# Kernel optimization log

Measured on AMD Instinct MI355X. Metric: run time of the kernel, lower is better.

Reference implementation:

```python
import jax, jax.numpy as jnp
import numpy as np

CR = 64                      # cond_repeat
DILS = tuple(2 ** i for _ in range(2) for i in range(10))  # 2 blocks x 10 layers
Q_ZERO = 128


def setup_inputs() -> dict:
    key = jax.random.key(0)
    B, C, TE = 8, 64, 8          # batch, cond channels, encoding timesteps
    R, S, Q = 128, 128, 256      # residual, skip, classes
    L = len(DILS)
    ks = jax.random.split(key, 12)
    sc = 0.1
    return {
        "encodings": jax.random.normal(ks[0], (B, C, TE), jnp.float32),
        "first_w": jax.random.normal(ks[1], (R, 1, 2), jnp.float32) * sc,
        "first_b": jnp.zeros((R,), jnp.float32),
        "causal_w": jax.random.normal(ks[2], (L, 2 * R, R, 2), jnp.float32) * sc,
        "causal_b": jnp.zeros((L, 2 * R), jnp.float32),
        "cond_w": jax.random.normal(ks[3], (L, 2 * R, C), jnp.float32) * sc,
        "cond_b": jnp.zeros((L, 2 * R), jnp.float32),
        "res_w": jax.random.normal(ks[4], (L, R, R), jnp.float32) * sc,
        "res_b": jnp.zeros((L, R), jnp.float32),
        "skip_w": jax.random.normal(ks[5], (L, S, R), jnp.float32) * sc,
        "skip_b": jnp.zeros((L, S), jnp.float32),
        "skipc_w": jax.random.normal(ks[6], (S, R), jnp.float32) * sc,
        "skipc_b": jnp.zeros((S,), jnp.float32),
        "fc_w": jax.random.normal(ks[7], (S, S), jnp.float32) * sc,
        "fc_b": jnp.zeros((S,), jnp.float32),
        "condf_w": jax.random.normal(ks[8], (S, C), jnp.float32) * sc,
        "condf_b": jnp.zeros((S,), jnp.float32),
        "logits_w": jax.random.normal(ks[9], (Q, S), jnp.float32) * sc,
        "logits_b": jnp.zeros((Q,), jnp.float32),
    }


def _generate(encodings, first_w, first_b, causal_w, causal_b, cond_w, cond_b,
              res_w, res_b, skip_w, skip_b, skipc_w, skipc_b, fc_w, fc_b,
              condf_w, condf_b, logits_w, logits_b):
    B = encodings.shape[0]
    R = res_w.shape[1]
    T = encodings.shape[2] * CR

    # ring buffers emulate QueuedConv1d (queue length = dilation, zero-initialized)
    buf_first0 = jnp.zeros((B, 1), jnp.float32)
    bufs0 = tuple(jnp.zeros((B, d, R), jnp.float32) for d in DILS)
    sample0 = jnp.full((B,), Q_ZERO, jnp.int32)

    def step(carry, t):
        sample, buf_first, bufs = carry
        x = sample.astype(jnp.float32) / 255.0 - 0.5                      # [B]
        c = jax.lax.dynamic_index_in_dim(encodings, t // CR, axis=2,
                                         keepdims=False)                  # [B,C]
        # first causal conv (1 -> R, kernel 2): tap0 on delayed sample, tap1 on current
        prev0 = buf_first[:, 0]
        buf_first = buf_first.at[:, 0].set(x)
        res = (prev0[:, None] * first_w[None, :, 0, 0]
               + x[:, None] * first_w[None, :, 0, 1] + first_b)           # [B,R]
        skip = res @ skipc_w.T + skipc_b                                  # [B,S]
        new_bufs = []
        for l, d in enumerate(DILS):
            idx = jnp.mod(t, d)
            prev = jax.lax.dynamic_index_in_dim(bufs[l], idx, axis=1, keepdims=False)
            new_bufs.append(jax.lax.dynamic_update_index_in_dim(bufs[l], res, idx, axis=1))
            z = (prev @ causal_w[l, :, :, 0].T + res @ causal_w[l, :, :, 1].T
                 + causal_b[l] + c @ cond_w[l].T + cond_b[l])             # [B,2R]
            gate, out = jnp.split(z, 2, axis=1)
            h = jax.nn.sigmoid(gate) * jnp.tanh(out)                      # [B,R]
            res = res + h @ res_w[l].T + res_b[l]
            skip = skip + h @ skip_w[l].T + skip_b[l]
        s = jax.nn.relu(skip) @ fc_w.T + fc_b + c @ condf_w.T + condf_b
        logits = jax.nn.relu(s) @ logits_w.T + logits_b                   # [B,Q]
        sample = jnp.argmax(logits, axis=1).astype(jnp.int32)             # 'max' sampling
        return (sample, buf_first, tuple(new_bufs)), (sample, logits)

    _, (samples, logits) = jax.lax.scan(step, (sample0, buf_first0, bufs0),
                                        jnp.arange(T))
    return samples, logits  # [T,B] int32, [T,B,Q] float32


def reference(encodings, first_w, first_b, causal_w, causal_b, cond_w, cond_b,
              res_w, res_b, skip_w, skip_b, skipc_w, skipc_b, fc_w, fc_b,
              condf_w, condf_b, logits_w, logits_b):
    return _generate(encodings, first_w, first_b, causal_w, causal_b, cond_w, cond_b,
                     res_w, res_b, skip_w, skip_b, skipc_w, skipc_b, fc_w, fc_b,
                     condf_w, condf_b, logits_w, logits_b)
```

## Files before the change

kernel.cpp:

```cpp
#include <hip/hip_runtime.h>
#include <math.h>

#define BB 8
#define TT 512
#define LL 20
#define NBLK 64
#define NTHR 256

typedef float f4 __attribute__((ext_vector_type(4)));
typedef unsigned long long ull;

__constant__ int c_dil[LL] = {1,2,4,8,16,32,64,128,256,512,
                              1,2,4,8,16,32,64,128,256,512};
__constant__ int c_roff[LL] = {-1,0,4096,12288,28672,61440,126976,258048,520192,1044480,
                               2093056,2095104,2099200,2107392,2123776,2156544,
                               2222080,2353152,2615296,3139584};

constexpr size_t OFF_RING = 0;
constexpr size_t OFF_X    = 4188160;

#define P_WC     0
#define P_F      20480
#define P_WST    30208
#define P_WSKIPC 30720
#define P_WFC    30976
#define P_WLOG   31232
#define P_WF0    31744
#define P_WF1    31872
#define P_FB     32000
#define P_CONDZ  32128
#define P_SFC    32768
#define P_RESB   32784
#define P_SKIPB  32824
#define P_ZB     32864
#define P_LOGB   32944
#define P_SKIPCB 32948
#define P_Z0C    32952
#define P_SKC    32976
#define P_XS     32984
#define P_SZ     33008
#define P_SL     33040
#define P_SKACC  33072
#define P_R2     33088
#define P_CF     33104
#define P_PREVF  33632
#define P_HF     34688
#define P_RESF   35744
#define P_RES0   36800
#define POOL_FL  37856

__device__ __forceinline__ f4 ldx(const f4* p) {
    f4 r;
    asm volatile("global_load_dwordx4 %0, %1, off sc0 sc1\n\ts_waitcnt vmcnt(0)"
                 : "=v"(r) : "v"(p) : "memory");
    return r;
}
__device__ __forceinline__ void ldx2(const f4* p0, const f4* p1, f4& a, f4& b) {
    asm volatile("global_load_dwordx4 %0, %2, off sc0 sc1\n\t"
                 "global_load_dwordx4 %1, %3, off sc0 sc1\n\t"
                 "s_waitcnt vmcnt(0)"
                 : "=v"(a), "=v"(b) : "v"(p0), "v"(p1) : "memory");
}
__device__ __forceinline__ void ld4x(const f4* a0, const f4* a1, const f4* a2, const f4* a3,
                                     f4& r0, f4& r1, f4& r2, f4& r3) {
    asm volatile("global_load_dwordx4 %0, %4, off sc0 sc1\n\t"
                 "global_load_dwordx4 %1, %5, off sc0 sc1\n\t"
                 "global_load_dwordx4 %2, %6, off sc0 sc1\n\t"
                 "global_load_dwordx4 %3, %7, off sc0 sc1\n\t"
                 "s_waitcnt vmcnt(0)"
                 : "=v"(r0), "=v"(r1), "=v"(r2), "=v"(r3)
                 : "v"(a0), "v"(a1), "v"(a2), "v"(a3) : "memory");
}
__device__ __forceinline__ void stx(f4* p, f4 v) {
    asm volatile("global_store_dwordx4 %0, %1, off sc0 sc1"
                 :: "v"(p), "v"(v) : "memory");
}
__device__ __forceinline__ void spin(const f4* p, int e, f4& a) {
    while (__float_as_int(a.w) != e) a = ldx(p);
}

__device__ __forceinline__ float pick16(const float* sl, int V) {
    if (V < 8) return sl[V];
    if (V >= 9 && V < 17) return sl[V - 1];
    return 0.f;
}
__device__ __forceinline__ void publish16(f4* slot, int J, const float* sl, int e) {
    if (threadIdx.x < 6) {
        int q = threadIdx.x;
        f4 v;
        v.x = pick16(sl, 3*q);
        v.y = pick16(sl, 3*q + 1);
        v.z = pick16(sl, 3*q + 2);
        v.w = __int_as_float(e);
        stx(slot + J*6 + q, v);
    }
}
__device__ __forceinline__ void publish_half(f4* slot, int J, int r, const float* half8,
                                             int e, int m) {
    int base = 3*m;
    f4 v;
    v.x = half8[base];
    v.y = (base + 1 < 8) ? half8[base + 1] : 0.f;
    v.z = (base + 2 < 8) ? half8[base + 2] : 0.f;
    v.w = __int_as_float(e);
    stx(slot + J*6 + 3*r + m, v);
}
__device__ __forceinline__ void scat16(float* dst, f4 v, int vi, bool dorelu) {
    int j = vi / 6, q = vi - 6*j;
    #pragma unroll
    for (int i = 0; i < 3; ++i) {
        int V = 3*q + i;
        float x = v[i];
        if (dorelu) x = fmaxf(x, 0.f);
        if (V < 8)                 dst[V*132 + 2*j]           = x;
        else if (V >= 9 && V < 17) dst[(V - 9)*132 + 2*j + 1] = x;
    }
}
__device__ __forceinline__ void consume16(const f4* slot, int e, float* dst, bool dorelu) {
    int m = threadIdx.x;
    const f4 *p0 = slot + m, *p1 = slot + 256 + m;
    f4 a, b;
    bool two = (m < 128);
    if (two) ldx2(p0, p1, a, b); else a = ldx(p0);
    spin(p0, e, a);
    if (two) spin(p1, e, b);
    scat16(dst, a, m, dorelu);
    if (two) scat16(dst, b, m + 256, dorelu);
}
__device__ __forceinline__ void consume_pair(const f4* sR, int eR, float* dR,
                                             const f4* sH, int eH, float* dH) {
    int m = threadIdx.x;
    const f4 *pra = sR + m, *prb = sR + 256 + m, *pha = sH + m, *phb = sH + 256 + m;
    f4 ra, rb, ha, hb;
    bool two = (m < 128);
    if (two) ld4x(pra, prb, pha, phb, ra, rb, ha, hb);
    else     ldx2(pra, pha, ra, ha);
    spin(pra, eR, ra);
    if (two) spin(prb, eR, rb);
    scat16(dR, ra, m, false);
    if (two) scat16(dR, rb, m + 256, false);
    spin(pha, eH, ha);
    if (two) spin(phb, eH, hb);
    scat16(dH, ha, m, false);
    if (two) scat16(dH, hb, m + 256, false);
}

__global__ __launch_bounds__(NTHR, 1) void wn_gen(
    const float* __restrict__ enc,
    const float* __restrict__ first_w,  const float* __restrict__ first_b,
    const float* __restrict__ causal_w, const float* __restrict__ causal_b,
    const float* __restrict__ cond_w,   const float* __restrict__ cond_b,
    const float* __restrict__ res_w,    const float* __restrict__ res_b,
    const float* __restrict__ skip_w,   const float* __restrict__ skip_b,
    const float* __restrict__ skipc_w,  const float* __restrict__ skipc_b,
    const float* __restrict__ fc_w,     const float* __restrict__ fc_b,
    const float* __restrict__ condf_w,  const float* __restrict__ condf_b,
    const float* __restrict__ logits_w, const float* __restrict__ logits_b,
    float* __restrict__ wsf, float* __restrict__ out)
{
    extern __shared__ float pool[];
    const int tid = threadIdx.x;
    const int J = blockIdx.x;
    float* ring = wsf + OFF_RING;
    f4* xb = (f4*)(wsf + OFF_X);

    for (int m = tid; m < 20480; m += NTHR) {
        int l = m >> 10, rem = m & 1023, g = rem >> 8, i = rem & 255;
        int grow = (g < 2) ? (2*J + g) : (128 + 2*J + (g - 2));
        int col = i & 127, k = i >> 7;
        pool[P_WC + m] = causal_w[((size_t)(l*256 + grow)*128 + col)*2 + k];
    }
    if (tid < 256) {
        int r = tid >> 7, i = tid & 127;
        pool[P_WSKIPC + tid] = skipc_w[(size_t)(2*J + r)*128 + i];
        pool[P_WFC + tid]    = fc_w[(size_t)(2*J + r)*128 + i];
    }
    for (int m = tid; m < 512; m += NTHR) {
        int w = m >> 7, i = m & 127;
        pool[P_WLOG + m] = logits_w[(size_t)(4*J + w)*128 + i];
    }
    if (tid < 128) {
        pool[P_WF0 + tid] = first_w[2*tid];
        pool[P_WF1 + tid] = first_w[2*tid + 1];
        pool[P_FB + tid]  = first_b[tid];
    }
    if (tid < 40) {
        int l = tid >> 1, r = tid & 1;
        pool[P_RESB + tid]  = res_b[l*128 + 2*J + r];
        pool[P_SKIPB + tid] = skip_b[l*128 + 2*J + r];
    }
    if (tid < 4) pool[P_LOGB + tid] = logits_b[4*J + tid];
    if (tid < 2) pool[P_SKIPCB + tid] = skipc_b[2*J + tid];
    if (tid < 8) {
        pool[P_XS + tid]      = 128.f/255.f - 0.5f;
        pool[P_XS + 8 + tid]  = 0.f;
        pool[P_XS + 16 + tid] = 0.f;
    }
    __syncthreads();

    for (int l = 0; l < 19; ++l) {
        for (int m = tid; m < 512; m += NTHR) {
            int g = m >> 7, j = m & 127;
            const float* w1 = pool + P_WC + ((l+1)*4 + g)*256 + 128;
            const float* rw = res_w + (size_t)l*128*128 + j;
            float acc = 0.f;
            #pragma unroll 8
            for (int i = 0; i < 128; ++i) acc += w1[i] * rw[(size_t)i*128];
            pool[P_F + (l*4 + g)*128 + j] = acc;
        }
    }
    if (tid < 80) {
        int l = tid >> 2, g = tid & 3;
        float acc = 0.f;
        if (l >= 1) {
            const float* w1 = pool + P_WC + (l*4 + g)*256 + 128;
            for (int i = 0; i < 128; ++i) acc += w1[i] * res_b[(l-1)*128 + i];
        }
        pool[P_ZB + tid] = acc;
    }
    if (tid < 4) {
        const float* w0 = pool + P_WC + tid*256;
        const float* w1 = w0 + 128;
        float kp = 0.f, kc = 0.f, u = 0.f, c1 = 0.f, a0 = 0.f;
        for (int j = 0; j < 128; ++j) {
            float f0 = pool[P_WF0 + j], f1 = pool[P_WF1 + j], fbv = pool[P_FB + j];
            kp += w0[j]*fbv; kc += w1[j]*fbv;
            u  += w0[j]*f0;  c1 += w0[j]*f1 + w1[j]*f0;  a0 += w1[j]*f1;
        }
        pool[P_Z0C + tid*6 + 0] = kp;
        pool[P_Z0C + tid*6 + 1] = kc;
        pool[P_Z0C + tid*6 + 2] = u;
        pool[P_Z0C + tid*6 + 3] = c1;
        pool[P_Z0C + tid*6 + 4] = a0;
    }
    if (tid < 2) {
        const float* wr = pool + P_WSKIPC + tid*128;
        float sk = pool[P_SKIPCB + tid], sa = 0.f, sb = 0.f;
        for (int j = 0; j < 128; ++j) {
            sk += wr[j]*pool[P_FB + j];
            sa += wr[j]*pool[P_WF0 + j];
            sb += wr[j]*pool[P_WF1 + j];
        }
        pool[P_SKC + tid*3 + 0] = sk;
        pool[P_SKC + tid*3 + 1] = sa;
        pool[P_SKC + tid*3 + 2] = sb;
    }
    __syncthreads();

    int e = 0;
    int er_pending = 0;
    int esk = 0;

    for (int t = 0; t < TT; ++t) {
        if ((t & 63) == 0) {
            int te = t >> 6;
            for (int m = tid; m < 512; m += NTHR) {
                int b = m >> 6, j = m & 63;
                pool[P_CF + b*66 + j] = enc[(size_t)b*512 + j*8 + te];
            }
            __syncthreads();
            for (int m = tid; m < 640; m += NTHR) {
                int l = m >> 5, rem = m & 31, g = rem >> 3, b = rem & 7;
                int grow = (g < 2) ? (2*J + g) : (128 + 2*J + (g - 2));
                float acc = causal_b[l*256 + grow] + cond_b[l*256 + grow]
                          + pool[P_ZB + l*4 + g];
                const float* cw = cond_w + (size_t)(l*256 + grow)*64;
                const float* cf = pool + P_CF + b*66;
                for (int j = 0; j < 64; ++j) acc += cw[j]*cf[j];
                pool[P_CONDZ + l*32 + g*8 + b] = acc;
            }
            if (tid < 16) {
                int r = tid >> 3, b = tid & 7, row = 2*J + r;
                float acc = fc_b[row] + condf_b[row];
                const float* cw = condf_w + (size_t)row*64;
                const float* cf = pool + P_CF + b*66;
                for (int j = 0; j < 64; ++j) acc += cw[j]*cf[j];
                pool[P_SFC + r*8 + b] = acc;
            }
            __syncthreads();
        }

        ++e; const int eh0 = e;
        {
            if (tid < 16) {
                int r = tid & 1, b = tid >> 1;
                float kf  = (t >= 1) ? 1.f : 0.f;
                float x0v = pool[P_XS + b];
                float x1v = pool[P_XS + 8 + b];
                float x2v = pool[P_XS + 16 + b];
                const float* zc = pool + P_Z0C;
                int g0 = r, g1 = 2 + r;
                float zg = kf*zc[g0*6+0] + zc[g0*6+1] + x2v*zc[g0*6+2]
                         + x1v*zc[g0*6+3] + x0v*zc[g0*6+4] + pool[P_CONDZ + g0*8 + b];
                float zo = kf*zc[g1*6+0] + zc[g1*6+1] + x2v*zc[g1*6+2]
                         + x1v*zc[g1*6+3] + x0v*zc[g1*6+4] + pool[P_CONDZ + g1*8 + b];
                pool[P_SL + r*8 + b] = (1.f/(1.f + expf(-zg))) * tanhf(zo);
            }
            publish16(xb + (size_t)(eh0 & 3)*768, J, pool + P_SL, eh0);
        }
        for (int m = tid; m < 1024; m += NTHR) {
            int b = m >> 7, r = m & 127;
            pool[P_RES0 + b*132 + r] =
                pool[P_FB + r] + pool[P_XS + 8 + b]*pool[P_WF0 + r]
                               + pool[P_XS + b]    *pool[P_WF1 + r];
        }
        if (tid < 16) {
            int r = tid >> 3, b = tid & 7;
            float x0v = pool[P_XS + b], x1v = pool[P_XS + 8 + b];
            pool[P_SKACC + r*8 + b] = pool[P_SKC + r*3] + x1v*pool[P_SKC + r*3 + 1]
                                                        + x0v*pool[P_SKC + r*3 + 2];
            int row = 2*J + r;
            pool[P_R2 + r*8 + b] = pool[P_FB + row] + x1v*pool[P_WF0 + row]
                                                    + x0v*pool[P_WF1 + row];
        }

        for (int l = 0; l < LL; ++l) {
            int ehh;
            if (l == 0) {
                ehh = eh0;
            } else {
                {
                    int g = tid >> 6, lane = tid & 63, b = lane >> 3, k = lane & 7;
                    const float* w0 = pool + P_WC + (l*4 + g)*256;
                    const float* pv = pool + P_PREVF + b*132;
                    const float* rs = ((l == 1) ? pool + P_RES0 : pool + P_RESF) + b*132;
                    const float* fm = pool + P_F + ((l-1)*4 + g)*128;
                    const float* hh = pool + P_HF + b*132;
                    float acc = 0.f;
                    #pragma unroll
                    for (int i = 0; i < 16; ++i) {
                        int j = k + 8*i;
                        acc += w0[j]*pv[j] + w0[128 + j]*rs[j] + fm[j]*hh[j];
                    }
                    acc += __shfl_xor(acc,1); acc += __shfl_xor(acc,2); acc += __shfl_xor(acc,4);
                    if (k == 0) pool[P_SZ + g*8 + b] = acc;
                }
                __syncthreads();
                ++e; ehh = e;
                if (tid < 16) {
                    int r = tid & 1, b = tid >> 1;
                    float g = pool[P_SZ + r*8 + b]     + pool[P_CONDZ + l*32 + r*8 + b];
                    float o = pool[P_SZ + (2+r)*8 + b] + pool[P_CONDZ + l*32 + (2+r)*8 + b];
                    pool[P_SL + r*8 + b] = (1.f/(1.f + expf(-g))) * tanhf(o);
                }
                publish16(xb + (size_t)(ehh & 3)*768, J, pool + P_SL, ehh);
            }
            float wv0, wv1;
            {
                int r0 = tid >> 7, i0 = tid & 127;
                wv0 = res_w [(size_t)(l*128 + 2*J + r0)*128 + i0];
                wv1 = skip_w[(size_t)(l*128 + 2*J + r0)*128 + i0];
            }
            ull pfa = 0, pfb = 0;
            if (l <= 18) {
                int d = c_dil[l+1];
                if (t >= d) {
                    int slot = (t - d) & (2*d - 1);
                    const float* rp = ring + c_roff[l+1] + (size_t)slot*1024 + tid*4;
                    pfa = __hip_atomic_load((const ull*)rp,     __ATOMIC_RELAXED, __HIP_MEMORY_SCOPE_AGENT);
                    pfb = __hip_atomic_load((const ull*)(rp+2), __ATOMIC_RELAXED, __HIP_MEMORY_SCOPE_AGENT);
                }
            }
            if (l == 0) {
                consume16(xb + (size_t)(ehh & 3)*768, ehh, pool + P_HF, false);
            } else if (l <= 18) {
                consume_pair(xb + (size_t)(er_pending & 3)*768, er_pending, pool + P_RESF,
                             xb + (size_t)(ehh & 3)*768,        ehh,        pool + P_HF);
            } else {
                consume16(xb + (size_t)(ehh & 3)*768, ehh, pool + P_HF, false);
            }
            pool[P_WST + tid] = wv0;
            pool[P_WST + 256 + tid] = wv1;
            __syncthreads();
            {
                int w = tid >> 6, lane = tid & 63, b = lane >> 3, k = lane & 7;
                int r = w & 1, isSkip = w >> 1;
                if (isSkip || l <= 18) {
                    const float* wr = pool + P_WST + (isSkip ? 256 : 0) + r*128;
                    const float* hh = pool + P_HF + b*132;
                    float acc = 0.f;
                    #pragma unroll
                    for (int i = 0; i < 16; ++i) { int j = k + 8*i; acc += wr[j]*hh[j]; }
                    acc += __shfl_xor(acc,1); acc += __shfl_xor(acc,2); acc += __shfl_xor(acc,4);
                    if (k == 0) {
                        if (isSkip) {
                            pool[P_SKACC + r*8 + b] += acc + pool[P_SKIPB + l*2 + r];
                        } else {
                            float v = pool[P_R2 + r*8 + b] + acc + pool[P_RESB + l*2 + r];
                            pool[P_R2 + r*8 + b] = v;
                            pool[P_SL + r*8 + b] = v;
                            int d = c_dil[l+1];
                            int slot = t & (2*d - 1);
                            float* wp = ring + c_roff[l+1] + (size_t)slot*1024 + b*128 + 2*J + r;
                            __hip_atomic_store(wp, v, __ATOMIC_RELAXED, __HIP_MEMORY_SCOPE_AGENT);
                        }
                    }
                }
            }
            {
                int w = tid >> 6, lane = tid & 63;
                if (l <= 17) {
                    ++e; er_pending = e;
                    if (w < 2 && lane < 3)
                        publish_half(xb + (size_t)(e & 3)*768, J, w,
                                     pool + P_SL + w*8, e, lane);
                } else if (l == 19) {
                    ++e; esk = e;
                    if (w >= 2 && lane < 3)
                        publish_half(xb + (size_t)(e & 3)*768, J, w - 2,
                                     pool + P_SKACC + (w - 2)*8, e, lane);
                }
            }
            if (l <= 18) {
                int b = tid >> 5, c = (tid & 31)*4;
                union { ull u; float f[2]; } u0, u1;
                u0.u = pfa; u1.u = pfb;
                float* dp = pool + P_PREVF + b*132 + c;
                dp[0] = u0.f[0]; dp[1] = u0.f[1]; dp[2] = u1.f[0]; dp[3] = u1.f[1];
            }
            __syncthreads();
        }

        consume16(xb + (size_t)(esk & 3)*768, esk, pool + P_HF, false);
        __syncthreads();
        {
            int w = tid >> 6, lane = tid & 63, b = lane >> 3, k = lane & 7;
            if (w < 2) {
                const float* wr = pool + P_WFC + w*128;
                const float* sk = pool + P_HF + b*132;
                float acc = 0.f;
                #pragma unroll
                for (int i = 0; i < 16; ++i) { int j = k + 8*i; acc += wr[j]*fmaxf(sk[j], 0.f); }
                acc += __shfl_xor(acc,1); acc += __shfl_xor(acc,2); acc += __shfl_xor(acc,4);
                if (k == 0) pool[P_SL + w*8 + b] = acc + pool[P_SFC + w*8 + b];
            }
        }
        ++e;
        {
            int w = tid >> 6, lane = tid & 63;
            if (w < 2 && lane < 3)
                publish_half(xb + (size_t)(e & 3)*768, J, w, pool + P_SL + w*8, e, lane);
        }
        consume16(xb + (size_t)(e & 3)*768, e, pool + P_RESF, true);
        __syncthreads();
        {
            int b = tid >> 5, g = (tid >> 3) & 3, k = tid & 7;
            const float* wr = pool + P_WLOG + g*128;
            const float* sv = pool + P_RESF + b*132;
            float acc = 0.f;
            #pragma unroll
            for (int i = 0; i < 16; ++i) { int j = k + 8*i; acc += wr[j]*sv[j]; }
            acc += __shfl_xor(acc,1); acc += __shfl_xor(acc,2); acc += __shfl_xor(acc,4);
            float v = acc + pool[P_LOGB + g];
            float best = (k == 0) ? v : -3.4e38f;
            int bi = 4*J + g;
            { float ov = __shfl_xor(best, 8);  int oi = __shfl_xor(bi, 8);
              if (ov > best || (ov == best && oi < bi)) { best = ov; bi = oi; } }
            { float ov = __shfl_xor(best, 16); int oi = __shfl_xor(bi, 16);
              if (ov > best || (ov == best && oi < bi)) { best = ov; bi = oi; } }
            if (k == 0) out[4096 + ((size_t)(t*BB + b))*256 + 4*J + g] = v;
            if ((tid & 31) == 0) { pool[P_SL + b] = best; pool[P_SL + 8 + b] = (float)bi; }
        }
        __syncthreads();
        ++e;
        publish16(xb + (size_t)(e & 3)*768, J, pool + P_SL, e);
        consume16(xb + (size_t)(e & 3)*768, e, pool + P_HF, false);
        __syncthreads();
        if (tid < 64) {
            int b = tid >> 3, j0 = tid & 7;
            float best = -3.4e38f; float bidx = 0.f;
            #pragma unroll
            for (int k2 = 0; k2 < 8; ++k2) {
                int j = j0*8 + k2;
                float v  = pool[P_HF + b*132 + 2*j];
                float id = pool[P_HF + b*132 + 2*j + 1];
                if (v > best || (v == best && id < bidx)) { best = v; bidx = id; }
            }
            #pragma unroll
            for (int m = 4; m >= 1; m >>= 1) {
                float ov = __shfl_xor(best, m); float oi = __shfl_xor(bidx, m);
                if (ov > best || (ov == best && oi < bidx)) { best = ov; bidx = oi; }
            }
            if (j0 == 0) {
                if (J == 0) out[t*BB + b] = bidx;
                pool[P_XS + 16 + b] = pool[P_XS + 8 + b];
                pool[P_XS + 8 + b]  = pool[P_XS + b];
                pool[P_XS + b]      = bidx*(1.f/255.f) - 0.5f;
            }
        }
        __syncthreads();
    }
}

extern "C" void kernel_launch(void* const* d_in, const int* in_sizes, int n_in,
                              void* d_out, int out_size, void* d_ws, size_t ws_size,
                              hipStream_t stream) {
    const float* enc      = (const float*)d_in[0];
    const float* first_w  = (const float*)d_in[1];
    const float* first_b  = (const float*)d_in[2];
    const float* causal_w = (const float*)d_in[3];
    const float* causal_b = (const float*)d_in[4];
    const float* cond_w   = (const float*)d_in[5];
    const float* cond_b   = (const float*)d_in[6];
    const float* res_w    = (const float*)d_in[7];
    const float* res_b    = (const float*)d_in[8];
    const float* skip_w   = (const float*)d_in[9];
    const float* skip_b   = (const float*)d_in[10];
    const float* skipc_w  = (const float*)d_in[11];
    const float* skipc_b  = (const float*)d_in[12];
    const float* fc_w     = (const float*)d_in[13];
    const float* fc_b     = (const float*)d_in[14];
    const float* condf_w  = (const float*)d_in[15];
    const float* condf_b  = (const float*)d_in[16];
    const float* logits_w = (const float*)d_in[17];
    const float* logits_b = (const float*)d_in[18];

    float* wsf = (float*)d_ws;
    float* out = (float*)d_out;

    wn_gen<<<NBLK, NTHR, POOL_FL*4, stream>>>(
        enc, first_w, first_b, causal_w, causal_b, cond_w, cond_b,
        res_w, res_b, skip_w, skip_b, skipc_w, skipc_b, fc_w, fc_b,
        condf_w, condf_b, logits_w, logits_b, wsf, out);
}
```

Measured before the change: 35.99 ms.

## Place all workers on one XCC so cross-block flags sync through L2 instead of L3

The kernel now launches 512 blocks and elects 64 of them that sit on XCC 0 using per-XCC atomic counters and a handshake with timeouts. If all 64 land on one XCC and agree, the spin-flag loads and stores drop the sc1 (system-coherent) bit, so the frequent inter-block messages stay in the shared L2. Otherwise it falls back to the original coherent path using the first 64 launched blocks. It also shrinks LDS by streaming causal weights per layer into a double buffer prefetched during the loop, instead of holding all layers. The cost is a more fragile election protocol, extra launched blocks, and timeout-based fallbacks.

```diff
diff --git a/kernel.cpp b/kernel.cpp
--- a/kernel.cpp
+++ b/kernel.cpp
@@ -4,11 +4,13 @@
 #define BB 8
 #define TT 512
 #define LL 20
-#define NBLK 64
 #define NTHR 256
+#define GRID 512
+#define WK 64
 
 typedef float f4 __attribute__((ext_vector_type(4)));
 typedef unsigned long long ull;
+typedef unsigned int u32;
 
 __constant__ int c_dil[LL] = {1,2,4,8,16,32,64,128,256,512,
                               1,2,4,8,16,32,64,128,256,512};
@@ -19,64 +21,114 @@
 constexpr size_t OFF_RING = 0;
 constexpr size_t OFF_X    = 4188160;
 
-#define P_WC     0
-#define P_F      20480
-#define P_WST    30208
-#define P_WSKIPC 30720
-#define P_WFC    30976
-#define P_WLOG   31232
-#define P_WF0    31744
-#define P_WF1    31872
-#define P_FB     32000
-#define P_CONDZ  32128
-#define P_SFC    32768
-#define P_RESB   32784
-#define P_SKIPB  32824
-#define P_ZB     32864
-#define P_LOGB   32944
-#define P_SKIPCB 32948
-#define P_Z0C    32952
-#define P_SKC    32976
-#define P_XS     32984
-#define P_SZ     33008
-#define P_SL     33040
-#define P_SKACC  33072
-#define P_R2     33088
-#define P_CF     33104
-#define P_PREVF  33632
-#define P_HF     34688
-#define P_RESF   35744
-#define P_RES0   36800
-#define POOL_FL  37856
-
-__device__ __forceinline__ f4 ldx(const f4* p) {
+__device__ ull g_seq;
+__device__ u32 g_xcnt[16];
+
+#define P_F      0
+#define P_WX     9728
+#define P_WST    11776
+#define P_WSKIPC 12288
+#define P_WFC    12544
+#define P_WLOG   12800
+#define P_WF0    13312
+#define P_WF1    13440
+#define P_FB     13568
+#define P_CONDZ  13696
+#define P_SFC    14336
+#define P_RESB   14352
+#define P_SKIPB  14392
+#define P_ZB     14432
+#define P_LOGB   14512
+#define P_SKIPCB 14516
+#define P_Z0C    14520
+#define P_SKC    14544
+#define P_XS     14552
+#define P_SZ     14576
+#define P_SL     14608
+#define P_SKACC  14640
+#define P_R2     14656
+#define P_CF     14672
+#define P_PREVF  15200
+#define P_HF     16256
+#define P_RESF   17312
+#define P_RES0   18368
+#define POOL_FL  19456
+
+template<bool L3S> __device__ __forceinline__ f4 ldx(const f4* p) {
     f4 r;
-    asm volatile("global_load_dwordx4 %0, %1, off sc0 sc1\n\ts_waitcnt vmcnt(0)"
+    if constexpr (L3S)
+        asm volatile("global_load_dwordx4 %0, %1, off sc0 sc1\n\ts_waitcnt vmcnt(0)"
+                     : "=v"(r) : "v"(p) : "memory");
+    else
+        asm volatile("global_load_dwordx4 %0, %1, off sc0\n\ts_waitcnt vmcnt(0)"
+                     : "=v"(r) : "v"(p) : "memory");
+    return r;
+}
+template<bool L3S> __device__ __forceinline__ void ldx2(const f4* p0, const f4* p1, f4& a, f4& b) {
+    if constexpr (L3S)
+        asm volatile("global_load_dwordx4 %0, %2, off sc0 sc1\n\t"
+                     "global_load_dwordx4 %1, %3, off sc0 sc1\n\t"
+                     "s_waitcnt vmcnt(0)"
+                     : "=&v"(a), "=&v"(b) : "v"(p0), "v"(p1) : "memory");
+    else
+        asm volatile("global_load_dwordx4 %0, %2, off sc0\n\t"
+                     "global_load_dwordx4 %1, %3, off sc0\n\t"
+                     "s_waitcnt vmcnt(0)"
+                     : "=&v"(a), "=&v"(b) : "v"(p0), "v"(p1) : "memory");
+}
+template<bool L3S> __device__ __forceinline__ void ld4x(const f4* a0, const f4* a1, const f4* a2, const f4* a3,
+                                                        f4& r0, f4& r1, f4& r2, f4& r3) {
+    if constexpr (L3S)
+        asm volatile("global_load_dwordx4 %0, %4, off sc0 sc1\n\t"
+                     "global_load_dwordx4 %1, %5, off sc0 sc1\n\t"
+                     "global_load_dwordx4 %2, %6, off sc0 sc1\n\t"
+                     "global_load_dwordx4 %3, %7, off sc0 sc1\n\t"
+                     "s_waitcnt vmcnt(0)"
+                     : "=&v"(r0), "=&v"(r1), "=&v"(r2), "=&v"(r3)
+                     : "v"(a0), "v"(a1), "v"(a2), "v"(a3) : "memory");
+    else
+        asm volatile("global_load_dwordx4 %0, %4, off sc0\n\t"
+                     "global_load_dwordx4 %1, %5, off sc0\n\t"
+                     "global_load_dwordx4 %2, %6, off sc0\n\t"
+                     "global_load_dwordx4 %3, %7, off sc0\n\t"
+                     "s_waitcnt vmcnt(0)"
+                     : "=&v"(r0), "=&v"(r1), "=&v"(r2), "=&v"(r3)
+                     : "v"(a0), "v"(a1), "v"(a2), "v"(a3) : "memory");
+}
+template<bool L3S> __device__ __forceinline__ void stx(f4* p, f4 v) {
+    if constexpr (L3S)
+        asm volatile("global_store_dwordx4 %0, %1, off sc0 sc1" :: "v"(p), "v"(v) : "memory");
+    else
+        asm volatile("global_store_dwordx4 %0, %1, off sc0" :: "v"(p), "v"(v) : "memory");
+}
+template<bool L3S> __device__ __forceinline__ void spin(const f4* p, int e, f4& a) {
+    while (__float_as_int(a.w) != e) a = ldx<L3S>(p);
+}
+
+__device__ __forceinline__ u32 ldw_l3(const u32* p) {
+    u32 r;
+    asm volatile("global_load_dword %0, %1, off sc0 sc1\n\ts_waitcnt vmcnt(0)"
                  : "=v"(r) : "v"(p) : "memory");
     return r;
 }
-__device__ __forceinline__ void ldx2(const f4* p0, const f4* p1, f4& a, f4& b) {
-    asm volatile("global_load_dwordx4 %0, %2, off sc0 sc1\n\t"
-                 "global_load_dwordx4 %1, %3, off sc0 sc1\n\t"
-                 "s_waitcnt vmcnt(0)"
-                 : "=v"(a), "=v"(b) : "v"(p0), "v"(p1) : "memory");
-}
-__device__ __forceinline__ void ld4x(const f4* a0, const f4* a1, const f4* a2, const f4* a3,
-                                     f4& r0, f4& r1, f4& r2, f4& r3) {
-    asm volatile("global_load_dwordx4 %0, %4, off sc0 sc1\n\t"
-                 "global_load_dwordx4 %1, %5, off sc0 sc1\n\t"
-                 "global_load_dwordx4 %2, %6, off sc0 sc1\n\t"
-                 "global_load_dwordx4 %3, %7, off sc0 sc1\n\t"
-                 "s_waitcnt vmcnt(0)"
-                 : "=v"(r0), "=v"(r1), "=v"(r2), "=v"(r3)
-                 : "v"(a0), "v"(a1), "v"(a2), "v"(a3) : "memory");
-}
-__device__ __forceinline__ void stx(f4* p, f4 v) {
-    asm volatile("global_store_dwordx4 %0, %1, off sc0 sc1"
+__device__ __forceinline__ void stw_l3(u32* p, u32 v) {
+    asm volatile("global_store_dword %0, %1, off sc0 sc1\n\ts_waitcnt vmcnt(0)"
                  :: "v"(p), "v"(v) : "memory");
 }
-__device__ __forceinline__ void spin(const f4* p, int e, f4& a) {
-    while (__float_as_int(a.w) != e) a = ldx(p);
+__device__ __forceinline__ u32 ldw_l2(const u32* p) {
+    u32 r;
+    asm volatile("global_load_dword %0, %1, off sc0\n\ts_waitcnt vmcnt(0)"
+                 : "=v"(r) : "v"(p) : "memory");
+    return r;
+}
+__device__ __forceinline__ void stw_l2(u32* p, u32 v) {
+    asm volatile("global_store_dword %0, %1, off sc0\n\ts_waitcnt vmcnt(0)"
+                 :: "v"(p), "v"(v) : "memory");
+}
+__device__ __forceinline__ ull rtime() {
+    ull t;
+    asm volatile("s_memrealtime %0\n\ts_waitcnt lgkmcnt(0)" : "=s"(t));
+    return t;
 }
 
 __device__ __forceinline__ float pick16(const float* sl, int V) {
@@ -84,7 +136,7 @@
     if (V >= 9 && V < 17) return sl[V - 1];
     return 0.f;
 }
-__device__ __forceinline__ void publish16(f4* slot, int J, const float* sl, int e) {
+template<bool L3S> __device__ __forceinline__ void publish16(f4* slot, int J, const float* sl, int e) {
     if (threadIdx.x < 6) {
         int q = threadIdx.x;
         f4 v;
@@ -92,18 +144,18 @@
         v.y = pick16(sl, 3*q + 1);
         v.z = pick16(sl, 3*q + 2);
         v.w = __int_as_float(e);
-        stx(slot + J*6 + q, v);
-    }
-}
-__device__ __forceinline__ void publish_half(f4* slot, int J, int r, const float* half8,
-                                             int e, int m) {
+        stx<L3S>(slot + J*6 + q, v);
+    }
+}
+template<bool L3S> __device__ __forceinline__ void publish_half(f4* slot, int J, int r, const float* half8,
+                                                                int e, int m) {
     int base = 3*m;
     f4 v;
     v.x = half8[base];
     v.y = (base + 1 < 8) ? half8[base + 1] : 0.f;
     v.z = (base + 2 < 8) ? half8[base + 2] : 0.f;
     v.w = __int_as_float(e);
-    stx(slot + J*6 + 3*r + m, v);
+    stx<L3S>(slot + J*6 + 3*r + m, v);
 }
 __device__ __forceinline__ void scat16(float* dst, f4 v, int vi, bool dorelu) {
     int j = vi / 6, q = vi - 6*j;
@@ -116,36 +168,41 @@
         else if (V >= 9 && V < 17) dst[(V - 9)*132 + 2*j + 1] = x;
     }
 }
-__device__ __forceinline__ void consume16(const f4* slot, int e, float* dst, bool dorelu) {
+template<bool L3S> __device__ __forceinline__ void consume16(const f4* slot, int e, float* dst, bool dorelu) {
     int m = threadIdx.x;
     const f4 *p0 = slot + m, *p1 = slot + 256 + m;
     f4 a, b;
     bool two = (m < 128);
-    if (two) ldx2(p0, p1, a, b); else a = ldx(p0);
-    spin(p0, e, a);
-    if (two) spin(p1, e, b);
+    if (two) ldx2<L3S>(p0, p1, a, b); else a = ldx<L3S>(p0);
+    spin<L3S>(p0, e, a);
+    if (two) spin<L3S>(p1, e, b);
     scat16(dst, a, m, dorelu);
     if (two) scat16(dst, b, m + 256, dorelu);
 }
-__device__ __forceinline__ void consume_pair(const f4* sR, int eR, float* dR,
-                                             const f4* sH, int eH, float* dH) {
+template<bool L3S> __device__ __forceinline__ void consume_pair(const f4* sR, int eR, float* dR,
+                                                                const f4* sH, int eH, float* dH) {
     int m = threadIdx.x;
     const f4 *pra = sR + m, *prb = sR + 256 + m, *pha = sH + m, *phb = sH + 256 + m;
     f4 ra, rb, ha, hb;
     bool two = (m < 128);
-    if (two) ld4x(pra, prb, pha, phb, ra, rb, ha, hb);
-    else     ldx2(pra, pha, ra, ha);
-    spin(pra, eR, ra);
-    if (two) spin(prb, eR, rb);
+    if (two) ld4x<L3S>(pra, prb, pha, phb, ra, rb, ha, hb);
+    else     ldx2<L3S>(pra, pha, ra, ha);
+    spin<L3S>(pra, eR, ra);
+    if (two) spin<L3S>(prb, eR, rb);
     scat16(dR, ra, m, false);
     if (two) scat16(dR, rb, m + 256, false);
-    spin(pha, eH, ha);
-    if (two) spin(phb, eH, hb);
+    spin<L3S>(pha, eH, ha);
+    if (two) spin<L3S>(phb, eH, hb);
     scat16(dH, ha, m, false);
     if (two) scat16(dH, hb, m + 256, false);
 }
 
-__global__ __launch_bounds__(NTHR, 1) void wn_gen(
+__device__ __forceinline__ int growf(int J, int g) {
+    return (g < 2) ? (2*J + g) : (128 + 2*J + (g - 2));
+}
+
+template<bool L3S>
+__device__ __attribute__((noinline)) void wn_body(const int J,
     const float* __restrict__ enc,
     const float* __restrict__ first_w,  const float* __restrict__ first_b,
     const float* __restrict__ causal_w, const float* __restrict__ causal_b,
@@ -160,17 +217,10 @@
 {
     extern __shared__ float pool[];
     const int tid = threadIdx.x;
-    const int J = blockIdx.x;
     float* ring = wsf + OFF_RING;
     f4* xb = (f4*)(wsf + OFF_X);
 
-    for (int m = tid; m < 20480; m += NTHR) {
-        int l = m >> 10, rem = m & 1023, g = rem >> 8, i = rem & 255;
-        int grow = (g < 2) ? (2*J + g) : (128 + 2*J + (g - 2));
-        int col = i & 127, k = i >> 7;
-        pool[P_WC + m] = causal_w[((size_t)(l*256 + grow)*128 + col)*2 + k];
-    }
-    if (tid < 256) {
+    {
         int r = tid >> 7, i = tid & 127;
         pool[P_WSKIPC + tid] = skipc_w[(size_t)(2*J + r)*128 + i];
         pool[P_WFC + tid]    = fc_w[(size_t)(2*J + r)*128 + i];
@@ -196,42 +246,28 @@
         pool[P_XS + 8 + tid]  = 0.f;
         pool[P_XS + 16 + tid] = 0.f;
     }
+    {
+        int g = tid >> 6, grow = growf(J, g);
+        f4 w = *(const f4*)(causal_w + (size_t)grow*256 + (tid & 63)*4);
+        *(f4*)&pool[P_WX + g*256 + (tid & 63)*4] = w;
+    }
     __syncthreads();
 
-    for (int l = 0; l < 19; ++l) {
-        for (int m = tid; m < 512; m += NTHR) {
-            int g = m >> 7, j = m & 127;
-            const float* w1 = pool + P_WC + ((l+1)*4 + g)*256 + 128;
-            const float* rw = res_w + (size_t)l*128*128 + j;
-            float acc = 0.f;
-            #pragma unroll 8
-            for (int i = 0; i < 128; ++i) acc += w1[i] * rw[(size_t)i*128];
-            pool[P_F + (l*4 + g)*128 + j] = acc;
-        }
-    }
-    if (tid < 80) {
-        int l = tid >> 2, g = tid & 3;
-        float acc = 0.f;
-        if (l >= 1) {
-            const float* w1 = pool + P_WC + (l*4 + g)*256 + 128;
-            for (int i = 0; i < 128; ++i) acc += w1[i] * res_b[(l-1)*128 + i];
-        }
-        pool[P_ZB + tid] = acc;
-    }
     if (tid < 4) {
-        const float* w0 = pool + P_WC + tid*256;
-        const float* w1 = w0 + 128;
+        const float* ws_ = pool + P_WX + tid*256;
         float kp = 0.f, kc = 0.f, u = 0.f, c1 = 0.f, a0 = 0.f;
         for (int j = 0; j < 128; ++j) {
+            float w0 = ws_[2*j], w1 = ws_[2*j + 1];
             float f0 = pool[P_WF0 + j], f1 = pool[P_WF1 + j], fbv = pool[P_FB + j];
-            kp += w0[j]*fbv; kc += w1[j]*fbv;
-            u  += w0[j]*f0;  c1 += w0[j]*f1 + w1[j]*f0;  a0 += w1[j]*f1;
+            kp += w0*fbv; kc += w1*fbv;
+            u  += w0*f0;  c1 += w0*f1 + w1*f0;  a0 += w1*f1;
         }
         pool[P_Z0C + tid*6 + 0] = kp;
         pool[P_Z0C + tid*6 + 1] = kc;
         pool[P_Z0C + tid*6 + 2] = u;
         pool[P_Z0C + tid*6 + 3] = c1;
         pool[P_Z0C + tid*6 + 4] = a0;
+        pool[P_ZB + tid] = 0.f;
     }
     if (tid < 2) {
         const float* wr = pool + P_WSKIPC + tid*128;
@@ -247,6 +283,31 @@
     }
     __syncthreads();
 
+    for (int l = 0; l < 19; ++l) {
+        {
+            int g = tid >> 6, grow = growf(J, g);
+            f4 w = *(const f4*)(causal_w + ((size_t)((l+1)*256 + grow))*256 + (tid & 63)*4);
+            *(f4*)&pool[P_WX + g*256 + (tid & 63)*4] = w;
+        }
+        __syncthreads();
+        for (int m = tid; m < 512; m += NTHR) {
+            int g = m >> 7, j = m & 127;
+            const float* w1 = pool + P_WX + g*256;
+            const float* rw = res_w + (size_t)l*128*128 + j;
+            float acc = 0.f;
+            #pragma unroll 8
+            for (int i = 0; i < 128; ++i) acc += w1[2*i + 1] * rw[(size_t)i*128];
+            pool[P_F + (l*4 + g)*128 + j] = acc;
+        }
+        if (tid < 4) {
+            const float* w1 = pool + P_WX + tid*256;
+            float acc = 0.f;
+            for (int i = 0; i < 128; ++i) acc += w1[2*i + 1] * res_b[l*128 + i];
+            pool[P_ZB + (l+1)*4 + tid] = acc;
+        }
+        __syncthreads();
+    }
+
     int e = 0;
     int er_pending = 0;
     int esk = 0;
@@ -261,7 +322,7 @@
             __syncthreads();
             for (int m = tid; m < 640; m += NTHR) {
                 int l = m >> 5, rem = m & 31, g = rem >> 3, b = rem & 7;
-                int grow = (g < 2) ? (2*J + g) : (128 + 2*J + (g - 2));
+                int grow = growf(J, g);
                 float acc = causal_b[l*256 + grow] + cond_b[l*256 + grow]
                           + pool[P_ZB + l*4 + g];
                 const float* cw = cond_w + (size_t)(l*256 + grow)*64;
@@ -296,7 +357,7 @@
                          + x1v*zc[g1*6+3] + x0v*zc[g1*6+4] + pool[P_CONDZ + g1*8 + b];
                 pool[P_SL + r*8 + b] = (1.f/(1.f + expf(-zg))) * tanhf(zo);
             }
-            publish16(xb + (size_t)(eh0 & 3)*768, J, pool + P_SL, eh0);
+            publish16<L3S>(xb + (size_t)(eh0 & 3)*768, J, pool + P_SL, eh0);
         }
         for (int m = tid; m < 1024; m += NTHR) {
             int b = m >> 7, r = m & 127;
@@ -321,7 +382,7 @@
             } else {
                 {
                     int g = tid >> 6, lane = tid & 63, b = lane >> 3, k = lane & 7;
-                    const float* w0 = pool + P_WC + (l*4 + g)*256;
+                    const float* wz = pool + P_WX + (l & 1)*1024 + g*256;
                     const float* pv = pool + P_PREVF + b*132;
                     const float* rs = ((l == 1) ? pool + P_RES0 : pool + P_RESF) + b*132;
                     const float* fm = pool + P_F + ((l-1)*4 + g)*128;
@@ -330,7 +391,7 @@
                     #pragma unroll
                     for (int i = 0; i < 16; ++i) {
                         int j = k + 8*i;
-                        acc += w0[j]*pv[j] + w0[128 + j]*rs[j] + fm[j]*hh[j];
+                        acc += wz[2*j]*pv[j] + wz[2*j + 1]*rs[j] + fm[j]*hh[j];
                     }
                     acc += __shfl_xor(acc,1); acc += __shfl_xor(acc,2); acc += __shfl_xor(acc,4);
                     if (k == 0) pool[P_SZ + g*8 + b] = acc;
@@ -343,13 +404,18 @@
                     float o = pool[P_SZ + (2+r)*8 + b] + pool[P_CONDZ + l*32 + (2+r)*8 + b];
                     pool[P_SL + r*8 + b] = (1.f/(1.f + expf(-g))) * tanhf(o);
                 }
-                publish16(xb + (size_t)(ehh & 3)*768, J, pool + P_SL, ehh);
+                publish16<L3S>(xb + (size_t)(ehh & 3)*768, J, pool + P_SL, ehh);
             }
             float wv0, wv1;
             {
                 int r0 = tid >> 7, i0 = tid & 127;
                 wv0 = res_w [(size_t)(l*128 + 2*J + r0)*128 + i0];
                 wv1 = skip_w[(size_t)(l*128 + 2*J + r0)*128 + i0];
+            }
+            f4 wcx;
+            if (l <= 18) {
+                int g = tid >> 6, grow = growf(J, g);
+                wcx = *(const f4*)(causal_w + ((size_t)((l+1)*256 + grow))*256 + (tid & 63)*4);
             }
             ull pfa = 0, pfb = 0;
             if (l <= 18) {
@@ -362,12 +428,12 @@
                 }
             }
             if (l == 0) {
-                consume16(xb + (size_t)(ehh & 3)*768, ehh, pool + P_HF, false);
+                consume16<L3S>(xb + (size_t)(ehh & 3)*768, ehh, pool + P_HF, false);
             } else if (l <= 18) {
-                consume_pair(xb + (size_t)(er_pending & 3)*768, er_pending, pool + P_RESF,
-                             xb + (size_t)(ehh & 3)*768,        ehh,        pool + P_HF);
+                consume_pair<L3S>(xb + (size_t)(er_pending & 3)*768, er_pending, pool + P_RESF,
+                                  xb + (size_t)(ehh & 3)*768,        ehh,        pool + P_HF);
             } else {
-                consume16(xb + (size_t)(ehh & 3)*768, ehh, pool + P_HF, false);
+                consume16<L3S>(xb + (size_t)(ehh & 3)*768, ehh, pool + P_HF, false);
             }
             pool[P_WST + tid] = wv0;
             pool[P_WST + 256 + tid] = wv1;
@@ -402,13 +468,13 @@
                 if (l <= 17) {
                     ++e; er_pending = e;
                     if (w < 2 && lane < 3)
-                        publish_half(xb + (size_t)(e & 3)*768, J, w,
-                                     pool + P_SL + w*8, e, lane);
+                        publish_half<L3S>(xb + (size_t)(e & 3)*768, J, w,
+                                          pool + P_SL + w*8, e, lane);
                 } else if (l == 19) {
                     ++e; esk = e;
                     if (w >= 2 && lane < 3)
-                        publish_half(xb + (size_t)(e & 3)*768, J, w - 2,
-                                     pool + P_SKACC + (w - 2)*8, e, lane);
+                        publish_half<L3S>(xb + (size_t)(e & 3)*768, J, w - 2,
+                                          pool + P_SKACC + (w - 2)*8, e, lane);
                 }
             }
             if (l <= 18) {
@@ -417,11 +483,12 @@
                 u0.u = pfa; u1.u = pfb;
                 float* dp = pool + P_PREVF + b*132 + c;
                 dp[0] = u0.f[0]; dp[1] = u0.f[1]; dp[2] = u1.f[0]; dp[3] = u1.f[1];
+                *(f4*)&pool[P_WX + ((l+1) & 1)*1024 + (tid >> 6)*256 + (tid & 63)*4] = wcx;
             }
             __syncthreads();
         }
 
-        consume16(xb + (size_t)(esk & 3)*768, esk, pool + P_HF, false);
+        consume16<L3S>(xb + (size_t)(esk & 3)*768, esk, pool + P_HF, false);
         __syncthreads();
         {
             int w = tid >> 6, lane = tid & 63, b = lane >> 3, k = lane & 7;
@@ -439,9 +506,9 @@
         {
             int w = tid >> 6, lane = tid & 63;
             if (w < 2 && lane < 3)
-                publish_half(xb + (size_t)(e & 3)*768, J, w, pool + P_SL + w*8, e, lane);
-        }
-        consume16(xb + (size_t)(e & 3)*768, e, pool + P_RESF, true);
+                publish_half<L3S>(xb + (size_t)(e & 3)*768, J, w, pool + P_SL + w*8, e, lane);
+        }
+        consume16<L3S>(xb + (size_t)(e & 3)*768, e, pool + P_RESF, true);
         __syncthreads();
         {
             int b = tid >> 5, g = (tid >> 3) & 3, k = tid & 7;
@@ -463,8 +530,8 @@
         }
         __syncthreads();
         ++e;
-        publish16(xb + (size_t)(e & 3)*768, J, pool + P_SL, e);
-        consume16(xb + (size_t)(e & 3)*768, e, pool + P_HF, false);
+        publish16<L3S>(xb + (size_t)(e & 3)*768, J, pool + P_SL, e);
+        consume16<L3S>(xb + (size_t)(e & 3)*768, e, pool + P_HF, false);
         __syncthreads();
         if (tid < 64) {
             int b = tid >> 3, j0 = tid & 7;
@@ -489,6 +556,129 @@
             }
         }
         __syncthreads();
+    }
+}
+
+__global__ __launch_bounds__(NTHR, 1) void wn_gen(
+    const float* __restrict__ enc,
+    const float* __restrict__ first_w,  const float* __restrict__ first_b,
+    const float* __restrict__ causal_w, const float* __restrict__ causal_b,
+    const float* __restrict__ cond_w,   const float* __restrict__ cond_b,
+    const float* __restrict__ res_w,    const float* __restrict__ res_b,
+    const float* __restrict__ skip_w,   const float* __restrict__ skip_b,
+    const float* __restrict__ skipc_w,  const float* __restrict__ skipc_b,
+    const float* __restrict__ fc_w,     const float* __restrict__ fc_b,
+    const float* __restrict__ condf_w,  const float* __restrict__ condf_b,
+    const float* __restrict__ logits_w, const float* __restrict__ logits_b,
+    float* __restrict__ wsf, float* __restrict__ out)
+{
+    extern __shared__ float pool[];
+    int* ip = (int*)pool;
+    const int tid = threadIdx.x;
+    u32* ex = (u32*)(wsf + OFF_X);
+
+    unsigned int xcc;
+    asm volatile("s_getreg_b32 %0, hwreg(HW_REG_XCC_ID)" : "=s"(xcc));
+    xcc &= 15u;
+
+    if (tid == 0) {
+        ull tk = atomicAdd(&g_seq, 1ull);
+        u32 tag = (u32)(tk >> 9) + 1u;
+        u32 idx = (u32)(tk & 511ull);
+        u32 rk;
+        {
+            u32* cp = &g_xcnt[xcc];
+            u32 old = __hip_atomic_load(cp, __ATOMIC_RELAXED, __HIP_MEMORY_SCOPE_AGENT);
+            while (true) {
+                u32 nv, mr;
+                if ((old >> 10) == tag) { mr = old & 1023u; nv = old + 1u; }
+                else                    { mr = 0u; nv = (tag << 10) | 1u; }
+                u32 prev = atomicCAS(cp, old, nv);
+                if (prev == old) { rk = mr; break; }
+                old = prev;
+            }
+        }
+        ip[0] = (int)tag; ip[1] = (int)idx; ip[2] = (int)rk;
+    }
+    __syncthreads();
+    const u32 tag = (u32)ip[0];
+    const u32 idx = (u32)ip[1];
+    const u32 rnk = (u32)ip[2];
+    const u32 hsh = tag * 0x9E3779B1u;
+    const bool primary = (xcc == 0u && rnk < (u32)WK);
+    const bool reserve = (idx < (u32)WK);
+
+    if (tid == 0) {
+        if (primary) stw_l3(ex + rnk, hsh);
+        if (idx == 0u) {
+            ull t0 = rtime(); int done = 0;
+            while (!done) {
+                int c = 0;
+                for (int j = 0; j < WK; ++j) c += (ldw_l3(ex + j) == hsh) ? 1 : 0;
+                done = (c == WK);
+                if (!done && (rtime() - t0) > 200000ull) break;
+            }
+            stw_l3(ex + 192, (hsh & ~3u) | (done ? 1u : 2u));
+        }
+        u32 verd = 2u;
+        ull t1 = rtime();
+        while (true) {
+            u32 v = ldw_l3(ex + 192);
+            if ((v & ~3u) == (hsh & ~3u)) { verd = v & 3u; break; }
+            if ((rtime() - t1) > 5000000ull) break;
+        }
+        ip[3] = (int)verd;
+    }
+    __syncthreads();
+    const u32 verd = (u32)ip[3];
+
+    if (verd == 1u) {
+        if (!primary) return;
+        const int J = (int)rnk;
+        if (tid == 0) {
+            stw_l2(ex + 64 + J, hsh);
+            ull t0 = rtime(); int ok = 0;
+            while (!ok) {
+                int c = 0;
+                for (int j = 0; j < WK; ++j) c += (ldw_l2(ex + 64 + j) == hsh) ? 1 : 0;
+                ok = (c == WK);
+                if (!ok && (rtime() - t0) > 200000ull) break;
+            }
+            stw_l3(ex + 128 + J, (hsh & ~1u) | (ok ? 1u : 0u));
+            if (J == 0) {
+                ull t1 = rtime(); int allok = 0;
+                while (!allok) {
+                    int c = 0;
+                    for (int j = 0; j < WK; ++j)
+                        c += (ldw_l3(ex + 128 + j) == ((hsh & ~1u) | 1u)) ? 1 : 0;
+                    allok = (c == WK);
+                    if (!allok && (rtime() - t1) > 400000ull) break;
+                }
+                stw_l3(ex + 193, (hsh & ~3u) | (allok ? 1u : 2u));
+            }
+            u32 fin = 2u;
+            ull t2 = rtime();
+            while (true) {
+                u32 v = ldw_l3(ex + 193);
+                if ((v & ~3u) == (hsh & ~3u)) { fin = v & 3u; break; }
+                if ((rtime() - t2) > 5000000ull) break;
+            }
+            ip[4] = (int)fin;
+        }
+        __syncthreads();
+        if (ip[4] == 1)
+            wn_body<false>(J, enc, first_w, first_b, causal_w, causal_b, cond_w, cond_b,
+                           res_w, res_b, skip_w, skip_b, skipc_w, skipc_b, fc_w, fc_b,
+                           condf_w, condf_b, logits_w, logits_b, wsf, out);
+        else
+            wn_body<true>(J, enc, first_w, first_b, causal_w, causal_b, cond_w, cond_b,
+                          res_w, res_b, skip_w, skip_b, skipc_w, skipc_b, fc_w, fc_b,
+                          condf_w, condf_b, logits_w, logits_b, wsf, out);
+    } else {
+        if (!reserve) return;
+        wn_body<true>((int)idx, enc, first_w, first_b, causal_w, causal_b, cond_w, cond_b,
+                      res_w, res_b, skip_w, skip_b, skipc_w, skipc_b, fc_w, fc_b,
+                      condf_w, condf_b, logits_w, logits_b, wsf, out);
     }
 }
 
@@ -518,7 +708,7 @@
     float* wsf = (float*)d_ws;
     float* out = (float*)d_out;
 
-    wn_gen<<<NBLK, NTHR, POOL_FL*4, stream>>>(
+    wn_gen<<<GRID, NTHR, POOL_FL*4, stream>>>(
         enc, first_w, first_b, causal_w, causal_b, cond_w, cond_b,
         res_w, res_b, skip_w, skip_b, skipc_w, skipc_b, fc_w, fc_b,
         condf_w, condf_b, logits_w, logits_b, wsf, out);
```

Result: slower. 43.78 ms (+21.7%).

## Remove per-layer barrier by fusing gate dot products and double-buffering H/res tiles

Applied to the files above, without the earlier changes.

The per-layer causal dot product, gate nonlinearity and publish now all run inside the first two wavefronts, each computing both gate and output rows with vectorized f4 loads. This removes one __syncthreads and the intermediate P_SZ scratch. The other two wavefronts handle the weight prefetch and ring-buffer prefetch with wider loads in parallel. H and residual buffers are double-buffered by layer parity so the next layer's consume can overwrite without a race. The cost is more shared memory, some load imbalance between wavefronts, and added complexity in the buffer-parity logic.

```diff
diff --git a/kernel.cpp b/kernel.cpp
--- a/kernel.cpp
+++ b/kernel.cpp
@@ -38,16 +38,14 @@
 #define P_Z0C    32952
 #define P_SKC    32976
 #define P_XS     32984
-#define P_SZ     33008
-#define P_SL     33040
-#define P_SKACC  33072
-#define P_R2     33088
-#define P_CF     33104
-#define P_PREVF  33632
-#define P_HF     34688
-#define P_RESF   35744
-#define P_RES0   36800
-#define POOL_FL  37856
+#define P_SL     33008
+#define P_SKACC  33040
+#define P_R2     33056
+#define P_CF     33072
+#define P_PREVF  33600
+#define P_HF     34656
+#define P_RESF   36768
+#define POOL_FL  38880
 
 __device__ __forceinline__ f4 ldx(const f4* p) {
     f4 r;
@@ -59,7 +57,7 @@
     asm volatile("global_load_dwordx4 %0, %2, off sc0 sc1\n\t"
                  "global_load_dwordx4 %1, %3, off sc0 sc1\n\t"
                  "s_waitcnt vmcnt(0)"
-                 : "=v"(a), "=v"(b) : "v"(p0), "v"(p1) : "memory");
+                 : "=&v"(a), "=&v"(b) : "v"(p0), "v"(p1) : "memory");
 }
 __device__ __forceinline__ void ld4x(const f4* a0, const f4* a1, const f4* a2, const f4* a3,
                                      f4& r0, f4& r1, f4& r2, f4& r3) {
@@ -68,7 +66,7 @@
                  "global_load_dwordx4 %2, %6, off sc0 sc1\n\t"
                  "global_load_dwordx4 %3, %7, off sc0 sc1\n\t"
                  "s_waitcnt vmcnt(0)"
-                 : "=v"(r0), "=v"(r1), "=v"(r2), "=v"(r3)
+                 : "=&v"(r0), "=&v"(r1), "=&v"(r2), "=&v"(r3)
                  : "v"(a0), "v"(a1), "v"(a2), "v"(a3) : "memory");
 }
 __device__ __forceinline__ void stx(f4* p, f4 v) {
@@ -143,6 +141,10 @@
     if (two) spin(phb, eH, hb);
     scat16(dH, ha, m, false);
     if (two) scat16(dH, hb, m + 256, false);
+}
+
+__device__ __forceinline__ float dotf4(f4 a, f4 b) {
+    return a.x*b.x + a.y*b.y + a.z*b.z + a.w*b.w;
 }
 
 __global__ __launch_bounds__(NTHR, 1) void wn_gen(
@@ -300,7 +302,7 @@
         }
         for (int m = tid; m < 1024; m += NTHR) {
             int b = m >> 7, r = m & 127;
-            pool[P_RES0 + b*132 + r] =
+            pool[P_RESF + b*132 + r] =
                 pool[P_FB + r] + pool[P_XS + 8 + b]*pool[P_WF0 + r]
                                + pool[P_XS + b]    *pool[P_WF1 + r];
         }
@@ -315,69 +317,79 @@
         }
 
         for (int l = 0; l < LL; ++l) {
+            const int par = l & 1;
+            const int w = tid >> 6, lane = tid & 63;
+            ull pf0 = 0, pf1 = 0, pf2 = 0, pf3 = 0;
             int ehh;
             if (l == 0) {
                 ehh = eh0;
             } else {
-                {
-                    int g = tid >> 6, lane = tid & 63, b = lane >> 3, k = lane & 7;
-                    const float* w0 = pool + P_WC + (l*4 + g)*256;
-                    const float* pv = pool + P_PREVF + b*132;
-                    const float* rs = ((l == 1) ? pool + P_RES0 : pool + P_RESF) + b*132;
-                    const float* fm = pool + P_F + ((l-1)*4 + g)*128;
-                    const float* hh = pool + P_HF + b*132;
-                    float acc = 0.f;
+                ++e; ehh = e;
+                if (w < 2) {
+                    int r = w, b = lane >> 3, k = lane & 7;
+                    const f4* wg = (const f4*)&pool[P_WC + (l*4 + r)*256];
+                    const f4* wo = (const f4*)&pool[P_WC + (l*4 + 2 + r)*256];
+                    const f4* fg = (const f4*)&pool[P_F + ((l-1)*4 + r)*128];
+                    const f4* fo = (const f4*)&pool[P_F + ((l-1)*4 + 2 + r)*128];
+                    const f4* pv = (const f4*)&pool[P_PREVF + b*132];
+                    const f4* rs = (const f4*)&pool[P_RESF + ((l-1) & 1)*1056 + b*132];
+                    const f4* hh = (const f4*)&pool[P_HF + ((l-1) & 1)*1056 + b*132];
+                    float ag = 0.f, ao = 0.f;
                     #pragma unroll
-                    for (int i = 0; i < 16; ++i) {
-                        int j = k + 8*i;
-                        acc += w0[j]*pv[j] + w0[128 + j]*rs[j] + fm[j]*hh[j];
+                    for (int i = 0; i < 4; ++i) {
+                        int j4 = k*4 + i;
+                        f4 p = pv[j4], rr = rs[j4], h = hh[j4];
+                        ag += dotf4(wg[j4], p) + dotf4(wg[32 + j4], rr) + dotf4(fg[j4], h);
+                        ao += dotf4(wo[j4], p) + dotf4(wo[32 + j4], rr) + dotf4(fo[j4], h);
                     }
-                    acc += __shfl_xor(acc,1); acc += __shfl_xor(acc,2); acc += __shfl_xor(acc,4);
-                    if (k == 0) pool[P_SZ + g*8 + b] = acc;
+                    ag += __shfl_xor(ag,1); ag += __shfl_xor(ag,2); ag += __shfl_xor(ag,4);
+                    ao += __shfl_xor(ao,1); ao += __shfl_xor(ao,2); ao += __shfl_xor(ao,4);
+                    if (k == 0) {
+                        float g = ag + pool[P_CONDZ + l*32 + r*8 + b];
+                        float o = ao + pool[P_CONDZ + l*32 + (2+r)*8 + b];
+                        pool[P_SL + r*8 + b] = (1.f/(1.f + expf(-g))) * tanhf(o);
+                    }
+                    if (lane < 3)
+                        publish_half(xb + (size_t)(ehh & 3)*768, J, r,
+                                     pool + P_SL + r*8, ehh, lane);
                 }
-                __syncthreads();
-                ++e; ehh = e;
-                if (tid < 16) {
-                    int r = tid & 1, b = tid >> 1;
-                    float g = pool[P_SZ + r*8 + b]     + pool[P_CONDZ + l*32 + r*8 + b];
-                    float o = pool[P_SZ + (2+r)*8 + b] + pool[P_CONDZ + l*32 + (2+r)*8 + b];
-                    pool[P_SL + r*8 + b] = (1.f/(1.f + expf(-g))) * tanhf(o);
+            }
+            if (w >= 2) {
+                int q = tid - 128;
+                int r0 = q >> 6, i0 = (q & 63)*2;
+                float2 v0 = *(const float2*)(res_w  + (size_t)(l*128 + 2*J + r0)*128 + i0);
+                float2 v1 = *(const float2*)(skip_w + (size_t)(l*128 + 2*J + r0)*128 + i0);
+                if (l <= 18) {
+                    int d = c_dil[l+1];
+                    if (t >= d) {
+                        int slot = (t - d) & (2*d - 1);
+                        const float* rp = ring + c_roff[l+1] + (size_t)slot*1024 + q*8;
+                        pf0 = __hip_atomic_load((const ull*)rp,     __ATOMIC_RELAXED, __HIP_MEMORY_SCOPE_AGENT);
+                        pf1 = __hip_atomic_load((const ull*)(rp+2), __ATOMIC_RELAXED, __HIP_MEMORY_SCOPE_AGENT);
+                        pf2 = __hip_atomic_load((const ull*)(rp+4), __ATOMIC_RELAXED, __HIP_MEMORY_SCOPE_AGENT);
+                        pf3 = __hip_atomic_load((const ull*)(rp+6), __ATOMIC_RELAXED, __HIP_MEMORY_SCOPE_AGENT);
+                    }
                 }
-                publish16(xb + (size_t)(ehh & 3)*768, J, pool + P_SL, ehh);
-            }
-            float wv0, wv1;
-            {
-                int r0 = tid >> 7, i0 = tid & 127;
-                wv0 = res_w [(size_t)(l*128 + 2*J + r0)*128 + i0];
-                wv1 = skip_w[(size_t)(l*128 + 2*J + r0)*128 + i0];
-            }
-            ull pfa = 0, pfb = 0;
-            if (l <= 18) {
-                int d = c_dil[l+1];
-                if (t >= d) {
-                    int slot = (t - d) & (2*d - 1);
-                    const float* rp = ring + c_roff[l+1] + (size_t)slot*1024 + tid*4;
-                    pfa = __hip_atomic_load((const ull*)rp,     __ATOMIC_RELAXED, __HIP_MEMORY_SCOPE_AGENT);
-                    pfb = __hip_atomic_load((const ull*)(rp+2), __ATOMIC_RELAXED, __HIP_MEMORY_SCOPE_AGENT);
-                }
+                *(float2*)&pool[P_WST + r0*128 + i0]       = v0;
+                *(float2*)&pool[P_WST + 256 + r0*128 + i0] = v1;
             }
             if (l == 0) {
                 consume16(xb + (size_t)(ehh & 3)*768, ehh, pool + P_HF, false);
             } else if (l <= 18) {
-                consume_pair(xb + (size_t)(er_pending & 3)*768, er_pending, pool + P_RESF,
-                             xb + (size_t)(ehh & 3)*768,        ehh,        pool + P_HF);
+                consume_pair(xb + (size_t)(er_pending & 3)*768, er_pending,
+                             pool + P_RESF + par*1056,
+                             xb + (size_t)(ehh & 3)*768, ehh,
+                             pool + P_HF + par*1056);
             } else {
-                consume16(xb + (size_t)(ehh & 3)*768, ehh, pool + P_HF, false);
-            }
-            pool[P_WST + tid] = wv0;
-            pool[P_WST + 256 + tid] = wv1;
+                consume16(xb + (size_t)(ehh & 3)*768, ehh, pool + P_HF + 1056, false);
+            }
             __syncthreads();
             {
-                int w = tid >> 6, lane = tid & 63, b = lane >> 3, k = lane & 7;
+                int b = lane >> 3, k = lane & 7;
                 int r = w & 1, isSkip = w >> 1;
                 if (isSkip || l <= 18) {
                     const float* wr = pool + P_WST + (isSkip ? 256 : 0) + r*128;
-                    const float* hh = pool + P_HF + b*132;
+                    const float* hh = pool + P_HF + par*1056 + b*132;
                     float acc = 0.f;
                     #pragma unroll
                     for (int i = 0; i < 16; ++i) { int j = k + 8*i; acc += wr[j]*hh[j]; }
@@ -398,7 +410,6 @@
                 }
             }
             {
-                int w = tid >> 6, lane = tid & 63;
                 if (l <= 17) {
                     ++e; er_pending = e;
                     if (w < 2 && lane < 3)
@@ -411,12 +422,13 @@
                                      pool + P_SKACC + (w - 2)*8, e, lane);
                 }
             }
-            if (l <= 18) {
-                int b = tid >> 5, c = (tid & 31)*4;
-                union { ull u; float f[2]; } u0, u1;
-                u0.u = pfa; u1.u = pfb;
+            if (w >= 2 && l <= 18) {
+                int q = tid - 128, b = q >> 4, c = (q & 15)*8;
+                union { ull u; float f[2]; } u0, u1, u2, u3;
+                u0.u = pf0; u1.u = pf1; u2.u = pf2; u3.u = pf3;
                 float* dp = pool + P_PREVF + b*132 + c;
                 dp[0] = u0.f[0]; dp[1] = u0.f[1]; dp[2] = u1.f[0]; dp[3] = u1.f[1];
+                dp[4] = u2.f[0]; dp[5] = u2.f[1]; dp[6] = u3.f[0]; dp[7] = u3.f[1];
             }
             __syncthreads();
         }
```

Result: slower. 36.86 ms (+2.4%).
